# Kernel tuning notes

Hardware: AMD Instinct MI355X
Metric: run time of the kernel (lower is better)

Reference implementation:

```python
import jax, jax.numpy as jnp
import numpy as np

# Dimensions: B graphs of NPG nodes each (equal sizes -> padding == reshape, exact)
B, NPG, DIN, H, E, DOUT, K_ORDER = 8, 4096, 128, 4, 262144, 128, 4
BETA = 0.5
N = B * NPG


def setup_inputs() -> dict:
    key = jax.random.key(0)
    k = jax.random.split(key, 12)
    s = 1.0 / np.sqrt(DIN)
    so = 1.0 / np.sqrt(H * DIN)
    x = jax.random.normal(k[0], (N, DIN), jnp.float32)
    Wq_w = jax.random.normal(k[1], (H * DIN, DIN), jnp.float32) * s
    Wq_b = jax.random.normal(k[2], (H * DIN,), jnp.float32) * 0.01
    Wk_w = jax.random.normal(k[3], (H * DIN, DIN), jnp.float32) * s
    Wk_b = jax.random.normal(k[4], (H * DIN,), jnp.float32) * 0.01
    Wo_w = jax.random.normal(k[5], (DOUT, H * DIN), jnp.float32) * so
    Wo_b = jax.random.normal(k[6], (DOUT,), jnp.float32) * 0.01
    # edges constrained within graphs (faithful to per-graph data)
    g = jax.random.randint(k[7], (E,), 0, B)
    row = g * NPG + jax.random.randint(k[8], (E,), 0, NPG)
    col = g * NPG + jax.random.randint(k[9], (E,), 0, NPG)
    edge_index = jnp.stack([row, col]).astype(jnp.int32)
    n_nodes = jnp.full((B,), NPG, jnp.int32)
    return {"x": x, "Wq_w": Wq_w, "Wq_b": Wq_b, "Wk_w": Wk_w, "Wk_b": Wk_b,
            "Wo_w": Wo_w, "Wo_b": Wo_b, "edge_index": edge_index, "n_nodes": n_nodes}


def _gcn(x, row, col):
    # x: [N,H,D]; symmetric-normalized message passing via segment sums
    deg = jax.ops.segment_sum(jnp.ones(row.shape[0], x.dtype), row, num_segments=N)
    safe = jnp.where(deg > 0, deg, 1.0)
    dis = jnp.where(deg > 0, safe ** -0.5, 0.0)
    w = (dis[row] * dis[col])[:, None, None]
    return jax.ops.segment_sum(x[col] * w, row, num_segments=N)


def _attn(qs, ks, v, n_f):
    # linear attention: out_i = (q_i . sum_j k_j v_j^T + sum_j v_j) / (q_i . sum_j k_j + n)
    q4 = qs.reshape(B, NPG, H, DIN)
    k4 = ks.reshape(B, NPG, H, DIN)
    v4 = v.reshape(B, NPG, H, DIN)
    kv = jnp.einsum('bnhd,bnhe->bhde', k4, v4)          # [B,H,D,D]
    ksum = k4.sum(axis=1)                                # [B,H,D]
    vsum = v4.sum(axis=1)                                # [B,H,D]
    num = jnp.einsum('bnhd,bhde->bnhe', q4, kv) + vsum[:, None]
    den = jnp.einsum('bnhd,bhd->bnh', q4, ksum) + n_f[:, None, None]
    return (num / den[..., None]).reshape(N, H, DIN)


def reference(x, Wq_w, Wq_b, Wk_w, Wk_b, Wo_w, Wo_b, edge_index, n_nodes):
    row, col = edge_index[0], edge_index[1]
    q = (x @ Wq_w.T + Wq_b).reshape(N, H, DIN)
    k = (x @ Wk_w.T + Wk_b).reshape(N, H, DIN)
    qs = q / jnp.linalg.norm(q, axis=2, keepdims=True)
    ks = k / jnp.linalg.norm(k, axis=2, keepdims=True)
    n_f = n_nodes.astype(x.dtype)
    xh = jnp.broadcast_to(x[:, None, :], (N, H, DIN))    # repeat over heads
    acc = xh
    cur = xh
    for _ in range(K_ORDER):
        cur = BETA * _gcn(cur, row, col) + (1.0 - BETA) * _attn(qs, ks, cur, n_f)
        acc = acc + cur
    xo = acc.reshape(N, H * DIN)
    return (xo @ Wo_w.T + Wo_b) / H
```

## Files before the change

kernel.cpp:

```cpp
#include <hip/hip_runtime.h>
#include <hip/hip_bf16.h>
#include <stdint.h>

typedef __hip_bfloat16 bf16;

#define BATCH  8
#define NPG    4096
#define DIN    128
#define NH     4
#define NEDGE  262144
#define DOUTF  128
#define KORDER 4
#define NTOT   (BATCH*NPG)
#define HD     (NH*DIN)

typedef __attribute__((ext_vector_type(8))) short short8;
typedef __attribute__((ext_vector_type(4))) float f32x4;

static __device__ __forceinline__ float b2f(bf16 v) { return __bfloat162float(v); }
static __device__ __forceinline__ float u2f(unsigned short u) {
    union { float f; unsigned int i; } c; c.i = ((unsigned int)u) << 16; return c.f;
}
static __device__ __forceinline__ unsigned short f2u(float f) {
    bf16 hb = __float2bfloat16(f);
    return *(unsigned short*)&hb;
}

__global__ void zero_kernel(uint4* p, int n) {
    int i = blockIdx.x * 256 + threadIdx.x;
    if (i < n) p[i] = uint4{0u, 0u, 0u, 0u};
}

__global__ void cvtbf_kernel(const float* __restrict__ in, bf16* __restrict__ out, int n) {
    int i = (blockIdx.x * 256 + threadIdx.x) * 8;
    if (i < n) {
        float4 a = *(const float4*)(in + i);
        float4 b = *(const float4*)(in + i + 4);
        unsigned short u[8] = { f2u(a.x), f2u(a.y), f2u(a.z), f2u(a.w),
                                f2u(b.x), f2u(b.y), f2u(b.z), f2u(b.w) };
        *(uint4*)(out + i) = *(uint4*)u;
    }
}

__global__ __launch_bounds__(256) void proj_mfma_kernel(const bf16* __restrict__ xbf,
                                                        const bf16* __restrict__ Wbf,
                                                        const float* __restrict__ bias,
                                                        bf16* __restrict__ outp,
                                                        bf16* __restrict__ outT) {
    __shared__ __align__(16) short t1[32][520];
    int n0 = blockIdx.x * 32;
    int tid = threadIdx.x;
    int lane = tid & 63, wc = tid >> 6;
    int l15 = lane & 15, quad = lane >> 4;

    f32x4 acc[2][8];
    #pragma unroll
    for (int i = 0; i < 2; i++)
        #pragma unroll
        for (int j = 0; j < 8; j++) acc[i][j] = f32x4{0.f, 0.f, 0.f, 0.f};

    #pragma unroll
    for (int ks = 0; ks < 4; ks++) {
        int kk = ks * 32 + quad * 8;
        short8 af[2];
        #pragma unroll
        for (int ti = 0; ti < 2; ti++)
            af[ti] = *(const short8*)(xbf + (size_t)(n0 + ti * 16 + l15) * DIN + kk);
        #pragma unroll
        for (int tj = 0; tj < 8; tj++) {
            short8 bfr = *(const short8*)(Wbf + (size_t)(wc * 128 + tj * 16 + l15) * DIN + kk);
            acc[0][tj] = __builtin_amdgcn_mfma_f32_16x16x32_bf16(af[0], bfr, acc[0][tj], 0, 0, 0);
            acc[1][tj] = __builtin_amdgcn_mfma_f32_16x16x32_bf16(af[1], bfr, acc[1][tj], 0, 0, 0);
        }
    }

    float bias_v[8];
    #pragma unroll
    for (int tj = 0; tj < 8; tj++) bias_v[tj] = bias[wc * 128 + tj * 16 + l15];

    #pragma unroll
    for (int ti = 0; ti < 2; ti++) {
        #pragma unroll
        for (int r = 0; r < 4; r++) {
            float s = 0.f;
            #pragma unroll
            for (int tj = 0; tj < 8; tj++) {
                float v = acc[ti][tj][r] + bias_v[tj];
                acc[ti][tj][r] = v;
                s += v * v;
            }
            s += __shfl_xor(s, 1); s += __shfl_xor(s, 2);
            s += __shfl_xor(s, 4); s += __shfl_xor(s, 8);
            float rs = rsqrtf(s);
            int node = ti * 16 + quad * 4 + r;
            #pragma unroll
            for (int tj = 0; tj < 8; tj++)
                t1[node][wc * 128 + tj * 16 + l15] = (short)f2u(acc[ti][tj][r] * rs);
        }
    }
    __syncthreads();

    if (outp) {
        #pragma unroll
        for (int u = 0; u < 8; u++) {
            int unit = u * 256 + tid;
            int nl = unit >> 6, fp = (unit & 63) * 8;
            *(uint4*)(outp + (size_t)(n0 + nl) * HD + fp) = *(uint4*)&t1[nl][fp];
        }
    }
    if (outT) {
        int b = n0 >> 12, nl0 = n0 & 4095;
        #pragma unroll
        for (int u = 0; u < 8; u++) {
            int unit = u * 256 + tid;
            int f = unit >> 2, np = (unit & 3) * 8;
            unsigned short arr[8];
            #pragma unroll
            for (int j = 0; j < 8; j++) arr[j] = (unsigned short)t1[np + j][f];
            *(uint4*)(outT + ((size_t)b * HD + f) * NPG + nl0 + np) = *(uint4*)arr;
        }
    }
}

__global__ void deg_kernel(const int* __restrict__ row, int* __restrict__ deg) {
    int e = blockIdx.x * 256 + threadIdx.x;
    if (e < NEDGE) atomicAdd(&deg[row[e]], 1);
}

__global__ void dis_kernel(const int* __restrict__ deg, float* __restrict__ dis) {
    int i = blockIdx.x * 256 + threadIdx.x;
    if (i < NTOT) {
        int d = deg[i];
        dis[i] = d > 0 ? rsqrtf((float)d) : 0.f;
    }
}

__global__ __launch_bounds__(1024) void scan1_kernel(const int* __restrict__ deg,
                                                     int* __restrict__ row_ptr, int* __restrict__ bsum) {
    __shared__ int buf[1024];
    int g = blockIdx.x, t = threadIdx.x;
    int v = deg[g * 1024 + t];
    buf[t] = v;
    __syncthreads();
    for (int off = 1; off < 1024; off <<= 1) {
        int add = (t >= off) ? buf[t - off] : 0;
        __syncthreads();
        buf[t] += add;
        __syncthreads();
    }
    row_ptr[g * 1024 + t] = buf[t] - v;
    if (t == 1023) bsum[g] = buf[1023];
}

__global__ void scan2_kernel(const int* __restrict__ bsum, int* __restrict__ boff, int* __restrict__ row_ptr) {
    int run = 0;
    for (int g = 0; g < 32; g++) { boff[g] = run; run += bsum[g]; }
    row_ptr[NTOT] = run;
}

__global__ __launch_bounds__(1024) void scan3_kernel(int* __restrict__ row_ptr, const int* __restrict__ boff) {
    row_ptr[blockIdx.x * 1024 + threadIdx.x] += boff[blockIdx.x];
}

__global__ __launch_bounds__(128) void sortperm_kernel(const int* __restrict__ row_ptr,
                                                       int* __restrict__ perm) {
    __shared__ int key[128];
    __shared__ int val[128];
    int tile = blockIdx.x;
    int t = threadIdx.x;
    int n = tile * 128 + t;
    key[t] = row_ptr[n + 1] - row_ptr[n];
    val[t] = t;
    __syncthreads();
    for (int k = 2; k <= 128; k <<= 1) {
        for (int j = k >> 1; j > 0; j >>= 1) {
            int ixj = t ^ j;
            if (ixj > t) {
                int a = key[t], b = key[ixj];
                bool up = ((t & k) == 0);
                if ((a > b) == up) {
                    key[t] = b; key[ixj] = a;
                    int va = val[t]; val[t] = val[ixj]; val[ixj] = va;
                }
            }
            __syncthreads();
        }
    }
    perm[tile * 128 + t] = val[t];
}

__global__ void scatter_kernel(const int* __restrict__ row, const int* __restrict__ col,
                               const int* __restrict__ row_ptr, int* __restrict__ fill,
                               const float* __restrict__ dis,
                               uint2* __restrict__ ecw) {
    int e = blockIdx.x * 256 + threadIdx.x;
    if (e < NEDGE) {
        int r = row[e], c = col[e];
        int pos = row_ptr[r] + atomicAdd(&fill[r], 1);
        ecw[pos] = uint2{(unsigned)c, __float_as_uint(dis[c])};
    }
}

__global__ __launch_bounds__(256) void rowsum_kernel(const bf16* __restrict__ T, float* __restrict__ out) {
    int row = blockIdx.x * 4 + (threadIdx.x >> 6);
    int lane = threadIdx.x & 63;
    const ushort4* p = (const ushort4*)(T + (size_t)row * NPG);
    float s = 0.f;
    #pragma unroll
    for (int wv = 0; wv < 16; wv++) {
        ushort4 u = p[lane + wv * 64];
        s += u2f(u.x) + u2f(u.y) + u2f(u.z) + u2f(u.w);
    }
    for (int off = 32; off > 0; off >>= 1) s += __shfl_down(s, off);
    if (lane == 0) out[row] = s;
}

__global__ __launch_bounds__(256) void colsum_kernel(const bf16* __restrict__ xbf, float* __restrict__ vsum) {
    __shared__ float buf[256];
    int b = blockIdx.x >> 3, sl = blockIdx.x & 7;
    int t = threadIdx.x;
    int d = t & 127, half = t >> 7;
    const unsigned short* p = (const unsigned short*)xbf + ((size_t)b * NPG + sl * 512 + half * 256) * DIN + d;
    float s = 0.f;
    for (int r = 0; r < 256; r++) s += u2f(p[(size_t)r * DIN]);
    buf[t] = s;
    __syncthreads();
    if (half == 0) {
        float tot = buf[d] + buf[d + 128];
        #pragma unroll
        for (int h = 0; h < NH; h++) atomicAdd(&vsum[b * HD + h * DIN + d], tot);
    }
}

__global__ __launch_bounds__(256) void den_kernel(const bf16* __restrict__ qs, const float* __restrict__ ksum,
                                                  const int* __restrict__ n_nodes, float* __restrict__ rden) {
    int n = blockIdx.x;
    int b = n >> 12;
    int w = threadIdx.x >> 6, lane = threadIdx.x & 63;
    int base = w * DIN;
    float p = b2f(qs[(size_t)n * HD + base + lane])      * ksum[b * HD + base + lane]
            + b2f(qs[(size_t)n * HD + base + 64 + lane]) * ksum[b * HD + base + 64 + lane];
    for (int off = 32; off > 0; off >>= 1) p += __shfl_down(p, off);
    if (lane == 0) rden[n * NH + w] = 1.0f / (p + (float)n_nodes[b]);
}

#define KVSPLIT 16
__global__ __launch_bounds__(512, 4) void kv_mfma_kernel(const bf16* __restrict__ ksT,
                                                         const bf16* __restrict__ vsrc,
                                                         int vld, int vhm,
                                                         float* __restrict__ partial) {
    __shared__ __align__(16) short kshT[128][72];
    __shared__ __align__(16) short vshT[128][72];
    int id = blockIdx.x;
    int b = id & 7;
    int u = id >> 3;
    int h = u >> 4;
    int s = u & 15;
    int bh = b * 4 + h;
    int blk = bh * KVSPLIT + s;
    int tid = threadIdx.x;
    int lane = tid & 63;
    int w = tid >> 6;
    int wr = w >> 1, wc = w & 1;
    int d0w = wr * 32, e0w = wc * 64;
    int l15 = lane & 15, quad = lane >> 4;

    f32x4 acc[2][4];
    #pragma unroll
    for (int i = 0; i < 2; i++)
        #pragma unroll
        for (int j = 0; j < 4; j++) acc[i][j] = f32x4{0.f, 0.f, 0.f, 0.f};

    const uint4* kg = (const uint4*)(ksT + ((size_t)bh * 128) * NPG);
    const bf16* vg = vsrc + (size_t)h * vhm;
    int n0 = s * (NPG / KVSPLIT);

    for (int c = 0; c < NPG / KVSPLIT / 64; c++) {
        int nb = n0 + c * 64;
        #pragma unroll
        for (int uu = 0; uu < 2; uu++) {
            int unit = uu * 512 + tid;
            int row = unit >> 3;
            int part = unit & 7;
            uint4 kd = kg[row * (NPG / 8) + (nb >> 3) + part];
            *(uint4*)&kshT[row][part * 8] = kd;
            int nl = unit >> 4;
            int fg = unit & 15;
            uint4 vd = *(const uint4*)(vg + (size_t)(b * NPG + nb + nl) * vld + fg * 8);
            unsigned short* sv = (unsigned short*)&vd;
            int ncol = nl ^ ((fg & 7) << 3);
            #pragma unroll
            for (int j = 0; j < 8; j++) vshT[fg * 8 + j][ncol] = (short)sv[j];
        }
        __syncthreads();
        #pragma unroll
        for (int kkstep = 0; kkstep < 2; kkstep++) {
            int kk = kkstep * 32 + quad * 8;
            short8 af[2], bfr[4];
            #pragma unroll
            for (int ti = 0; ti < 2; ti++)
                af[ti] = *(const short8*)&kshT[d0w + ti * 16 + l15][kk];
            #pragma unroll
            for (int tj = 0; tj < 4; tj++) {
                int e = e0w + tj * 16 + l15;
                bfr[tj] = *(const short8*)&vshT[e][kk ^ (((e >> 3) & 7) << 3)];
            }
            #pragma unroll
            for (int ti = 0; ti < 2; ti++)
                #pragma unroll
                for (int tj = 0; tj < 4; tj++)
                    acc[ti][tj] = __builtin_amdgcn_mfma_f32_16x16x32_bf16(af[ti], bfr[tj], acc[ti][tj], 0, 0, 0);
        }
        __syncthreads();
    }
    float* p = partial + (size_t)blk * (128 * 128);
    #pragma unroll
    for (int ti = 0; ti < 2; ti++)
        #pragma unroll
        for (int tj = 0; tj < 4; tj++)
            #pragma unroll
            for (int r = 0; r < 4; r++) {
                int row = d0w + ti * 16 + quad * 4 + r;
                int col = e0w + tj * 16 + l15;
                p[row * 128 + col] = acc[ti][tj][r];
            }
}

__global__ __launch_bounds__(256) void kvredB_kernel(const float* __restrict__ partial, bf16* __restrict__ kvB) {
    __shared__ __align__(16) short t[16][136];
    int blk = blockIdx.x;
    int bh = blk >> 3;
    int e0 = (blk & 7) * 16;
    int tid = threadIdx.x;
    int el = tid & 15;
    int dc = tid >> 4;
    const float* p = partial + (size_t)bh * (KVSPLIT * 16384);
    #pragma unroll
    for (int j = 0; j < 8; j++) {
        int d = dc * 8 + j;
        int idx = d * 128 + e0 + el;
        float s = 0.f;
        #pragma unroll
        for (int sl = 0; sl < KVSPLIT; sl++) s += p[sl * 16384 + idx];
        t[el][d] = (short)f2u(s);
    }
    __syncthreads();
    int e = tid >> 4, dp = (tid & 15) * 8;
    *(uint4*)((unsigned short*)kvB + (size_t)bh * 16384 + (e0 + e) * 128 + dp) = *(uint4*)&t[e][dp];
}

static __device__ __forceinline__ void acc8(float* g, uint4 v, float w) {
    unsigned short* sv = (unsigned short*)&v;
    #pragma unroll
    for (int k = 0; k < 8; k++) g[k] += w * u2f(sv[k]);
}

#define EMAX 1536
__global__ __launch_bounds__(512, 2) void gcn_attn_kernel(const bf16* __restrict__ qs,
                                                          const bf16* __restrict__ kvB,
                                                          const bf16* __restrict__ gsrc,
                                                          int gld, int ghm,
                                                          const int* __restrict__ row_ptr,
                                                          const int* __restrict__ perm,
                                                          const uint2* __restrict__ ecw,
                                                          const float* __restrict__ dis,
                                                          const float* __restrict__ vsum,
                                                          const float* __restrict__ rden,
                                                          bf16* __restrict__ curN,
                                                          float* __restrict__ vsumN) {
    __shared__ __align__(16) short t1[128][136];
    __shared__ __align__(8) uint2 est[EMAX];
    int id = blockIdx.x;
    int b = id & 7;
    int u = id >> 3;
    int h = u >> 5;
    int m = u & 31;
    int bh = b * 4 + h;
    int n0 = b * NPG + m * 128;
    int tid = threadIdx.x;
    int lane = tid & 63, w = tid >> 6;
    int wr = w >> 1, wc = w & 1;
    int e0w = wc * 64;
    int l15 = lane & 15, quad = lane >> 4;

    int ebase = row_ptr[n0];
    int ecnt = row_ptr[n0 + 128] - ebase;
    int scnt = ecnt < EMAX ? ecnt : EMAX;
    for (int i = tid; i < scnt; i += 512) est[i] = ecw[ebase + i];
    __syncthreads();

    {
        int nl = perm[n0 + (tid >> 2)];
        int sub = tid & 3;
        int n = n0 + nl;
        int start = row_ptr[n] - ebase;
        int end   = row_ptr[n + 1] - ebase;
        int lend  = end < scnt ? end : scnt;
        float g[32];
        #pragma unroll
        for (int i = 0; i < 32; i++) g[i] = 0.f;
        const bf16* gbase = gsrc + (size_t)h * ghm + sub * 32;

        int cA = 0, cB = 0; float wA = 0.f, wB = 0.f;
        if (start < lend)     { uint2 p = est[start];     cA = (int)p.x; wA = __uint_as_float(p.y); }
        if (start + 1 < lend) { uint2 p = est[start + 1]; cB = (int)p.x; wB = __uint_as_float(p.y); }
        uint4 vA0, vA1, vA2, vA3, vB0, vB1, vB2, vB3;
        {
            const uint4* p = (const uint4*)(gbase + (size_t)cA * gld);
            vA0 = p[0]; vA1 = p[1]; vA2 = p[2]; vA3 = p[3];
        }
        {
            const uint4* p = (const uint4*)(gbase + (size_t)cB * gld);
            vB0 = p[0]; vB1 = p[1]; vB2 = p[2]; vB3 = p[3];
        }
        for (int j = start; j < lend; j += 2) {
            int cC = 0, cD = 0; float wC = 0.f, wD = 0.f;
            if (j + 2 < lend) { uint2 p = est[j + 2]; cC = (int)p.x; wC = __uint_as_float(p.y); }
            if (j + 3 < lend) { uint2 p = est[j + 3]; cD = (int)p.x; wD = __uint_as_float(p.y); }
            acc8(g +  0, vA0, wA); acc8(g +  8, vA1, wA);
            acc8(g + 16, vA2, wA); acc8(g + 24, vA3, wA);
            {
                const uint4* p = (const uint4*)(gbase + (size_t)cC * gld);
                vA0 = p[0]; vA1 = p[1]; vA2 = p[2]; vA3 = p[3];
            }
            acc8(g +  0, vB0, wB); acc8(g +  8, vB1, wB);
            acc8(g + 16, vB2, wB); acc8(g + 24, vB3, wB);
            {
                const uint4* p = (const uint4*)(gbase + (size_t)cD * gld);
                vB0 = p[0]; vB1 = p[1]; vB2 = p[2]; vB3 = p[3];
            }
            wA = wC; wB = wD;
        }
        int fstart = start > lend ? start : lend;
        for (int j = fstart; j < end; j++) {
            uint2 pe = ecw[ebase + j];
            int c = (int)pe.x; float ww = __uint_as_float(pe.y);
            const uint4* p = (const uint4*)(gbase + (size_t)c * gld);
            acc8(g +  0, p[0], ww); acc8(g +  8, p[1], ww);
            acc8(g + 16, p[2], ww); acc8(g + 24, p[3], ww);
        }

        float dn = dis[n];
        int sw = (nl >> 3) & 7;
        #pragma unroll
        for (int q = 0; q < 4; q++) {
            unsigned short arr[8];
            #pragma unroll
            for (int k = 0; k < 8; k++) arr[k] = f2u(g[q * 8 + k] * dn);
            int fb = (sub * 4 + q) ^ sw;
            *(uint4*)&t1[nl][fb * 8] = *(uint4*)arr;
        }
    }

    f32x4 acc[2][4];
    #pragma unroll
    for (int i = 0; i < 2; i++)
        #pragma unroll
        for (int j = 0; j < 4; j++) acc[i][j] = f32x4{0.f, 0.f, 0.f, 0.f};

    const bf16* Aq = qs + (size_t)n0 * HD + h * DIN;
    const unsigned short* Bk = (const unsigned short*)kvB + (size_t)bh * 16384;
    #pragma unroll
    for (int ks = 0; ks < 4; ks++) {
        int kk = ks * 32 + quad * 8;
        short8 af[2], bfr[4];
        #pragma unroll
        for (int ti = 0; ti < 2; ti++)
            af[ti] = *(const short8*)(Aq + (size_t)(wr * 32 + ti * 16 + l15) * HD + kk);
        #pragma unroll
        for (int tj = 0; tj < 4; tj++)
            bfr[tj] = *(const short8*)(Bk + (e0w + tj * 16 + l15) * 128 + kk);
        #pragma unroll
        for (int ti = 0; ti < 2; ti++)
            #pragma unroll
            for (int tj = 0; tj < 4; tj++)
                acc[ti][tj] = __builtin_amdgcn_mfma_f32_16x16x32_bf16(af[ti], bfr[tj], acc[ti][tj], 0, 0, 0);
    }
    __syncthreads();

    #pragma unroll
    for (int tj = 0; tj < 4; tj++) {
        int el = e0w + tj * 16 + l15;
        float vs = vsum[b * HD + h * DIN + el];
        float cs = 0.f;
        #pragma unroll
        for (int ti = 0; ti < 2; ti++) {
            int nlb = wr * 32 + ti * 16 + quad * 4;
            #pragma unroll
            for (int r = 0; r < 4; r++) {
                int nl = nlb + r;
                int sw = (nl >> 3) & 7;
                int pc = (((el >> 3) ^ sw) * 8) | (el & 7);
                float attnv = (acc[ti][tj][r] + vs) * rden[(size_t)(n0 + nl) * NH + h];
                float g = u2f((unsigned short)t1[nl][pc]);
                float val = 0.5f * g + 0.5f * attnv;
                t1[nl][pc] = (short)f2u(val);
                cs += val;
            }
        }
        cs += __shfl_xor(cs, 16);
        cs += __shfl_xor(cs, 32);
        if (quad == 0) atomicAdd(&vsumN[b * HD + h * DIN + el], cs);
    }
    __syncthreads();

    {
        bf16* dstn = curN + (size_t)n0 * HD + h * DIN;
        #pragma unroll
        for (int uu = 0; uu < 4; uu++) {
            int unit = uu * 512 + tid;
            int nl = unit >> 4, fb = unit & 15;
            int sw = (nl >> 3) & 7;
            uint4 v = *(uint4*)&t1[nl][(fb ^ sw) * 8];
            *(uint4*)(dstn + (size_t)nl * HD + fb * 8) = v;
        }
    }
}

__global__ __launch_bounds__(256, 4) void out_mfma_kernel(const bf16* __restrict__ xbf,
                                                          const bf16* __restrict__ c1,
                                                          const bf16* __restrict__ c2,
                                                          const bf16* __restrict__ c3,
                                                          const bf16* __restrict__ c4,
                                                          const bf16* __restrict__ Wobf,
                                                          const float* __restrict__ Wo_b,
                                                          float* __restrict__ out) {
    __shared__ __align__(16) short ash[32][520];
    int n0 = blockIdx.x * 32;
    int tid = threadIdx.x;
    int lane = tid & 63, w = tid >> 6;
    int l15 = lane & 15, quad = lane >> 4;

    #pragma unroll 4
    for (int uu = 0; uu < 8; uu++) {
        int unit = uu * 256 + tid;
        int row = unit >> 6, cg = unit & 63;
        int col = cg * 8;
        size_t rbase = (size_t)(n0 + row);
        uint4 vx = *(const uint4*)(xbf + rbase * DIN + (col & 127));
        uint4 v1 = *(const uint4*)(c1 + rbase * HD + col);
        uint4 v2 = *(const uint4*)(c2 + rbase * HD + col);
        uint4 v3 = *(const uint4*)(c3 + rbase * HD + col);
        uint4 v4 = *(const uint4*)(c4 + rbase * HD + col);
        unsigned short* px = (unsigned short*)&vx;
        unsigned short* p1 = (unsigned short*)&v1;
        unsigned short* p2 = (unsigned short*)&v2;
        unsigned short* p3 = (unsigned short*)&v3;
        unsigned short* p4 = (unsigned short*)&v4;
        unsigned short o[8];
        #pragma unroll
        for (int j = 0; j < 8; j++)
            o[j] = f2u(u2f(px[j]) + u2f(p1[j]) + u2f(p2[j]) + u2f(p3[j]) + u2f(p4[j]));
        *(uint4*)&ash[row][col] = *(uint4*)o;
    }
    __syncthreads();

    f32x4 acc[2][2];
    #pragma unroll
    for (int i = 0; i < 2; i++)
        #pragma unroll
        for (int j = 0; j < 2; j++) acc[i][j] = f32x4{0.f, 0.f, 0.f, 0.f};

    #pragma unroll
    for (int ks = 0; ks < 16; ks++) {
        int kk = ks * 32 + quad * 8;
        short8 af[2], bfr[2];
        #pragma unroll
        for (int ti = 0; ti < 2; ti++)
            af[ti] = *(const short8*)&ash[ti * 16 + l15][kk];
        #pragma unroll
        for (int tj = 0; tj < 2; tj++)
            bfr[tj] = *(const short8*)(Wobf + (size_t)(w * 32 + tj * 16 + l15) * HD + kk);
        #pragma unroll
        for (int ti = 0; ti < 2; ti++)
            #pragma unroll
            for (int tj = 0; tj < 2; tj++)
                acc[ti][tj] = __builtin_amdgcn_mfma_f32_16x16x32_bf16(af[ti], bfr[tj], acc[ti][tj], 0, 0, 0);
    }

    #pragma unroll
    for (int tj = 0; tj < 2; tj++) {
        int col = w * 32 + tj * 16 + l15;
        float bv = Wo_b[col];
        #pragma unroll
        for (int ti = 0; ti < 2; ti++) {
            int rowb = ti * 16 + quad * 4;
            #pragma unroll
            for (int r = 0; r < 4; r++)
                out[(size_t)(n0 + rowb + r) * DOUTF + col] = (acc[ti][tj][r] + bv) * 0.25f;
        }
    }
}

extern "C" void kernel_launch(void* const* d_in, const int* in_sizes, int n_in,
                              void* d_out, int out_size, void* d_ws, size_t ws_size,
                              hipStream_t stream) {
    const float* x     = (const float*)d_in[0];
    const float* Wq_w  = (const float*)d_in[1];
    const float* Wq_b  = (const float*)d_in[2];
    const float* Wk_w  = (const float*)d_in[3];
    const float* Wk_b  = (const float*)d_in[4];
    const float* Wo_w  = (const float*)d_in[5];
    const float* Wo_b  = (const float*)d_in[6];
    const int*   edge  = (const int*)d_in[7];
    const int*   n_nod = (const int*)d_in[8];
    float* out = (float*)d_out;
    const int* erow = edge;
    const int* ecol = edge + NEDGE;

    char* w = (char*)d_ws;
    auto alloc = [&](size_t bytes) -> char* {
        char* p = w;
        w += (bytes + 255) & ~(size_t)255;
        return p;
    };
    bf16*  qs      = (bf16*) alloc((size_t)NTOT * HD * 2);
    bf16*  ksT     = (bf16*) alloc((size_t)NTOT * HD * 2);
    bf16*  cur1    = (bf16*) alloc((size_t)NTOT * HD * 2);
    bf16*  cur2    = (bf16*) alloc((size_t)NTOT * HD * 2);
    bf16*  cur3    = (bf16*) alloc((size_t)NTOT * HD * 2);
    bf16*  cur4    = (bf16*) alloc((size_t)NTOT * HD * 2);
    bf16*  xbf     = (bf16*) alloc((size_t)NTOT * DIN * 2);
    float* partial = (float*)alloc((size_t)32 * KVSPLIT * 16384 * 4);
    bf16*  kvB     = (bf16*) alloc((size_t)32 * 16384 * 2);
    bf16*  Wobf    = (bf16*) alloc(DOUTF * HD * 2);
    int*   degfill = (int*)  alloc(2 * NTOT * 4);
    float* dis     = (float*)alloc(NTOT * 4);
    int*   row_ptr = (int*)  alloc((NTOT + 1) * 4);
    int*   perm    = (int*)  alloc(NTOT * 4);
    uint2* ecw     = (uint2*)alloc((size_t)NEDGE * 8);
    float* ksum    = (float*)alloc(BATCH * HD * 4);
    float* vsumA   = (float*)alloc(BATCH * HD * 4);
    float* vsumB   = (float*)alloc(BATCH * HD * 4);
    float* rden    = (float*)alloc((size_t)NTOT * NH * 4);
    int*   bsum    = (int*)  alloc(32 * 4);
    int*   boff    = (int*)  alloc(32 * 4);
    int* deg  = degfill;
    int* fill = degfill + NTOT;
    bf16* Wqbf = (bf16*)partial;
    bf16* Wkbf = Wqbf + (size_t)HD * DIN;

    zero_kernel<<<64, 256, 0, stream>>>((uint4*)degfill, 2 * NTOT / 4);

    cvtbf_kernel<<<NTOT * DIN / 8 / 256, 256, 0, stream>>>(x, xbf, NTOT * DIN);
    cvtbf_kernel<<<HD * DIN / 8 / 256, 256, 0, stream>>>(Wq_w, Wqbf, HD * DIN);
    cvtbf_kernel<<<HD * DIN / 8 / 256, 256, 0, stream>>>(Wk_w, Wkbf, HD * DIN);
    cvtbf_kernel<<<DOUTF * HD / 8 / 256, 256, 0, stream>>>(Wo_w, Wobf, DOUTF * HD);

    proj_mfma_kernel<<<NTOT / 32, 256, 0, stream>>>(xbf, Wqbf, Wq_b, qs, (bf16*)nullptr);
    proj_mfma_kernel<<<NTOT / 32, 256, 0, stream>>>(xbf, Wkbf, Wk_b, (bf16*)nullptr, ksT);

    deg_kernel<<<NEDGE / 256, 256, 0, stream>>>(erow, deg);
    dis_kernel<<<NTOT / 256, 256, 0, stream>>>(deg, dis);
    scan1_kernel<<<32, 1024, 0, stream>>>(deg, row_ptr, bsum);
    scan2_kernel<<<1, 1, 0, stream>>>(bsum, boff, row_ptr);
    scan3_kernel<<<32, 1024, 0, stream>>>(row_ptr, boff);
    sortperm_kernel<<<NTOT / 128, 128, 0, stream>>>(row_ptr, perm);
    scatter_kernel<<<NEDGE / 256, 256, 0, stream>>>(erow, ecol, row_ptr, fill, dis, ecw);

    rowsum_kernel<<<BATCH * HD / 4, 256, 0, stream>>>(ksT, ksum);
    den_kernel<<<NTOT, 256, 0, stream>>>(qs, ksum, n_nod, rden);

    zero_kernel<<<4, 256, 0, stream>>>((uint4*)vsumA, BATCH * HD / 4);
    colsum_kernel<<<64, 256, 0, stream>>>(xbf, vsumA);

    bf16* curs[4] = { cur1, cur2, cur3, cur4 };
    float* vs = vsumA;
    float* vsN = vsumB;
    for (int it = 0; it < KORDER; it++) {
        const bf16* src = (it == 0) ? xbf : curs[it - 1];
        int ld = (it == 0) ? DIN : HD;
        int hm = (it == 0) ? 0 : DIN;
        kv_mfma_kernel<<<32 * KVSPLIT, 512, 0, stream>>>(ksT, src, ld, hm, partial);
        kvredB_kernel<<<256, 256, 0, stream>>>(partial, kvB);
        zero_kernel<<<4, 256, 0, stream>>>((uint4*)vsN, BATCH * HD / 4);
        gcn_attn_kernel<<<32 * 32, 512, 0, stream>>>(qs, kvB, src, ld, hm, row_ptr, perm, ecw, dis,
                                                     vs, rden, curs[it], vsN);
        float* tf = vs; vs = vsN; vsN = tf;
    }

    out_mfma_kernel<<<NTOT / 32, 256, 0, stream>>>(xbf, cur1, cur2, cur3, cur4, Wobf, Wo_b, out);

    (void)in_sizes; (void)n_in; (void)out_size; (void)ws_size;
}
```

Baseline: 565.0 us.

## Halve gcn_attn node tile to 64 rows and fold vsum zeroing into kvred

Reworks the fused GCN+attention kernel to process 64 nodes per block instead of 128. The grid doubles to 2048 blocks, with 8 threads per node each gathering 16 features and one MFMA row-tile per wave. Sortperm and the shared edge-stage buffer shrink to match. The separate zero_kernel launch for the next vsum buffer is folded into an extra block of kvredB. The aim is more parallelism and less per-thread register pressure in the gather, plus one fewer launch per iteration, at the cost of more per-block overhead, more vsum atomics and kvB reloads.

Result: slower. 632.7 us (+12.0%).

```diff
diff --git a/kernel.cpp b/kernel.cpp
--- a/kernel.cpp
+++ b/kernel.cpp
@@ -162,17 +162,17 @@
     row_ptr[blockIdx.x * 1024 + threadIdx.x] += boff[blockIdx.x];
 }
 
-__global__ __launch_bounds__(128) void sortperm_kernel(const int* __restrict__ row_ptr,
-                                                       int* __restrict__ perm) {
-    __shared__ int key[128];
-    __shared__ int val[128];
+__global__ __launch_bounds__(64) void sortperm_kernel(const int* __restrict__ row_ptr,
+                                                      int* __restrict__ perm) {
+    __shared__ int key[64];
+    __shared__ int val[64];
     int tile = blockIdx.x;
     int t = threadIdx.x;
-    int n = tile * 128 + t;
+    int n = tile * 64 + t;
     key[t] = row_ptr[n + 1] - row_ptr[n];
     val[t] = t;
     __syncthreads();
-    for (int k = 2; k <= 128; k <<= 1) {
+    for (int k = 2; k <= 64; k <<= 1) {
         for (int j = k >> 1; j > 0; j >>= 1) {
             int ixj = t ^ j;
             if (ixj > t) {
@@ -186,7 +186,7 @@
             __syncthreads();
         }
     }
-    perm[tile * 128 + t] = val[t];
+    perm[tile * 64 + t] = val[t];
 }
 
 __global__ void scatter_kernel(const int* __restrict__ row, const int* __restrict__ col,
@@ -326,7 +326,15 @@
             }
 }
 
-__global__ __launch_bounds__(256) void kvredB_kernel(const float* __restrict__ partial, bf16* __restrict__ kvB) {
+__global__ __launch_bounds__(256) void kvredB_kernel(const float* __restrict__ partial, bf16* __restrict__ kvB,
+                                                     float* __restrict__ vsumN) {
+    if (blockIdx.x == 256) {
+        ((uint4*)vsumN)[threadIdx.x] = uint4{0u, 0u, 0u, 0u};
+        ((uint4*)vsumN)[256 + threadIdx.x] = uint4{0u, 0u, 0u, 0u};
+        ((uint4*)vsumN)[512 + threadIdx.x] = uint4{0u, 0u, 0u, 0u};
+        ((uint4*)vsumN)[768 + threadIdx.x] = uint4{0u, 0u, 0u, 0u};
+        return;
+    }
     __shared__ __align__(16) short t[16][136];
     int blk = blockIdx.x;
     int bh = blk >> 3;
@@ -355,7 +363,7 @@
     for (int k = 0; k < 8; k++) g[k] += w * u2f(sv[k]);
 }
 
-#define EMAX 1536
+#define EMAX 1024
 __global__ __launch_bounds__(512, 2) void gcn_attn_kernel(const bf16* __restrict__ qs,
                                                           const bf16* __restrict__ kvB,
                                                           const bf16* __restrict__ gsrc,
@@ -368,15 +376,15 @@
                                                           const float* __restrict__ rden,
                                                           bf16* __restrict__ curN,
                                                           float* __restrict__ vsumN) {
-    __shared__ __align__(16) short t1[128][136];
+    __shared__ __align__(16) short t1[64][136];
     __shared__ __align__(8) uint2 est[EMAX];
     int id = blockIdx.x;
     int b = id & 7;
     int u = id >> 3;
-    int h = u >> 5;
-    int m = u & 31;
+    int h = u >> 6;
+    int m = u & 63;
     int bh = b * 4 + h;
-    int n0 = b * NPG + m * 128;
+    int n0 = b * NPG + m * 64;
     int tid = threadIdx.x;
     int lane = tid & 63, w = tid >> 6;
     int wr = w >> 1, wc = w & 1;
@@ -384,50 +392,48 @@
     int l15 = lane & 15, quad = lane >> 4;
 
     int ebase = row_ptr[n0];
-    int ecnt = row_ptr[n0 + 128] - ebase;
+    int ecnt = row_ptr[n0 + 64] - ebase;
     int scnt = ecnt < EMAX ? ecnt : EMAX;
     for (int i = tid; i < scnt; i += 512) est[i] = ecw[ebase + i];
     __syncthreads();
 
     {
-        int nl = perm[n0 + (tid >> 2)];
-        int sub = tid & 3;
+        int nl = perm[n0 + (tid >> 3)];
+        int sub = tid & 7;
         int n = n0 + nl;
         int start = row_ptr[n] - ebase;
         int end   = row_ptr[n + 1] - ebase;
         int lend  = end < scnt ? end : scnt;
-        float g[32];
-        #pragma unroll
-        for (int i = 0; i < 32; i++) g[i] = 0.f;
-        const bf16* gbase = gsrc + (size_t)h * ghm + sub * 32;
+        float g[16];
+        #pragma unroll
+        for (int i = 0; i < 16; i++) g[i] = 0.f;
+        const bf16* gbase = gsrc + (size_t)h * ghm + sub * 16;
 
         int cA = 0, cB = 0; float wA = 0.f, wB = 0.f;
         if (start < lend)     { uint2 p = est[start];     cA = (int)p.x; wA = __uint_as_float(p.y); }
         if (start + 1 < lend) { uint2 p = est[start + 1]; cB = (int)p.x; wB = __uint_as_float(p.y); }
-        uint4 vA0, vA1, vA2, vA3, vB0, vB1, vB2, vB3;
+        uint4 vA0, vA1, vB0, vB1;
         {
             const uint4* p = (const uint4*)(gbase + (size_t)cA * gld);
-            vA0 = p[0]; vA1 = p[1]; vA2 = p[2]; vA3 = p[3];
+            vA0 = p[0]; vA1 = p[1];
         }
         {
             const uint4* p = (const uint4*)(gbase + (size_t)cB * gld);
-            vB0 = p[0]; vB1 = p[1]; vB2 = p[2]; vB3 = p[3];
+            vB0 = p[0]; vB1 = p[1];
         }
         for (int j = start; j < lend; j += 2) {
             int cC = 0, cD = 0; float wC = 0.f, wD = 0.f;
             if (j + 2 < lend) { uint2 p = est[j + 2]; cC = (int)p.x; wC = __uint_as_float(p.y); }
             if (j + 3 < lend) { uint2 p = est[j + 3]; cD = (int)p.x; wD = __uint_as_float(p.y); }
-            acc8(g +  0, vA0, wA); acc8(g +  8, vA1, wA);
-            acc8(g + 16, vA2, wA); acc8(g + 24, vA3, wA);
+            acc8(g + 0, vA0, wA); acc8(g + 8, vA1, wA);
             {
                 const uint4* p = (const uint4*)(gbase + (size_t)cC * gld);
-                vA0 = p[0]; vA1 = p[1]; vA2 = p[2]; vA3 = p[3];
+                vA0 = p[0]; vA1 = p[1];
             }
-            acc8(g +  0, vB0, wB); acc8(g +  8, vB1, wB);
-            acc8(g + 16, vB2, wB); acc8(g + 24, vB3, wB);
+            acc8(g + 0, vB0, wB); acc8(g + 8, vB1, wB);
             {
                 const uint4* p = (const uint4*)(gbase + (size_t)cD * gld);
-                vB0 = p[0]; vB1 = p[1]; vB2 = p[2]; vB3 = p[3];
+                vB0 = p[0]; vB1 = p[1];
             }
             wA = wC; wB = wD;
         }
@@ -436,45 +442,38 @@
             uint2 pe = ecw[ebase + j];
             int c = (int)pe.x; float ww = __uint_as_float(pe.y);
             const uint4* p = (const uint4*)(gbase + (size_t)c * gld);
-            acc8(g +  0, p[0], ww); acc8(g +  8, p[1], ww);
-            acc8(g + 16, p[2], ww); acc8(g + 24, p[3], ww);
+            acc8(g + 0, p[0], ww); acc8(g + 8, p[1], ww);
         }
 
         float dn = dis[n];
         int sw = (nl >> 3) & 7;
         #pragma unroll
-        for (int q = 0; q < 4; q++) {
+        for (int q = 0; q < 2; q++) {
             unsigned short arr[8];
             #pragma unroll
             for (int k = 0; k < 8; k++) arr[k] = f2u(g[q * 8 + k] * dn);
-            int fb = (sub * 4 + q) ^ sw;
+            int fb = (sub * 2 + q) ^ sw;
             *(uint4*)&t1[nl][fb * 8] = *(uint4*)arr;
         }
     }
 
-    f32x4 acc[2][4];
-    #pragma unroll
-    for (int i = 0; i < 2; i++)
-        #pragma unroll
-        for (int j = 0; j < 4; j++) acc[i][j] = f32x4{0.f, 0.f, 0.f, 0.f};
+    f32x4 acc[4];
+    #pragma unroll
+    for (int j = 0; j < 4; j++) acc[j] = f32x4{0.f, 0.f, 0.f, 0.f};
 
     const bf16* Aq = qs + (size_t)n0 * HD + h * DIN;
     const unsigned short* Bk = (const unsigned short*)kvB + (size_t)bh * 16384;
     #pragma unroll
     for (int ks = 0; ks < 4; ks++) {
         int kk = ks * 32 + quad * 8;
-        short8 af[2], bfr[4];
-        #pragma unroll
-        for (int ti = 0; ti < 2; ti++)
-            af[ti] = *(const short8*)(Aq + (size_t)(wr * 32 + ti * 16 + l15) * HD + kk);
+        short8 af = *(const short8*)(Aq + (size_t)(wr * 16 + l15) * HD + kk);
+        short8 bfr[4];
         #pragma unroll
         for (int tj = 0; tj < 4; tj++)
             bfr[tj] = *(const short8*)(Bk + (e0w + tj * 16 + l15) * 128 + kk);
         #pragma unroll
-        for (int ti = 0; ti < 2; ti++)
-            #pragma unroll
-            for (int tj = 0; tj < 4; tj++)
-                acc[ti][tj] = __builtin_amdgcn_mfma_f32_16x16x32_bf16(af[ti], bfr[tj], acc[ti][tj], 0, 0, 0);
+        for (int tj = 0; tj < 4; tj++)
+            acc[tj] = __builtin_amdgcn_mfma_f32_16x16x32_bf16(af, bfr[tj], acc[tj], 0, 0, 0);
     }
     __syncthreads();
 
@@ -483,20 +482,17 @@
         int el = e0w + tj * 16 + l15;
         float vs = vsum[b * HD + h * DIN + el];
         float cs = 0.f;
-        #pragma unroll
-        for (int ti = 0; ti < 2; ti++) {
-            int nlb = wr * 32 + ti * 16 + quad * 4;
-            #pragma unroll
-            for (int r = 0; r < 4; r++) {
-                int nl = nlb + r;
-                int sw = (nl >> 3) & 7;
-                int pc = (((el >> 3) ^ sw) * 8) | (el & 7);
-                float attnv = (acc[ti][tj][r] + vs) * rden[(size_t)(n0 + nl) * NH + h];
-                float g = u2f((unsigned short)t1[nl][pc]);
-                float val = 0.5f * g + 0.5f * attnv;
-                t1[nl][pc] = (short)f2u(val);
-                cs += val;
-            }
+        int nlb = wr * 16 + quad * 4;
+        #pragma unroll
+        for (int r = 0; r < 4; r++) {
+            int nl = nlb + r;
+            int sw = (nl >> 3) & 7;
+            int pc = (((el >> 3) ^ sw) * 8) | (el & 7);
+            float attnv = (acc[tj][r] + vs) * rden[(size_t)(n0 + nl) * NH + h];
+            float g = u2f((unsigned short)t1[nl][pc]);
+            float val = 0.5f * g + 0.5f * attnv;
+            t1[nl][pc] = (short)f2u(val);
+            cs += val;
         }
         cs += __shfl_xor(cs, 16);
         cs += __shfl_xor(cs, 32);
@@ -507,7 +503,7 @@
     {
         bf16* dstn = curN + (size_t)n0 * HD + h * DIN;
         #pragma unroll
-        for (int uu = 0; uu < 4; uu++) {
+        for (int uu = 0; uu < 2; uu++) {
             int unit = uu * 512 + tid;
             int nl = unit >> 4, fb = unit & 15;
             int sw = (nl >> 3) & 7;
@@ -655,7 +651,7 @@
     scan1_kernel<<<32, 1024, 0, stream>>>(deg, row_ptr, bsum);
     scan2_kernel<<<1, 1, 0, stream>>>(bsum, boff, row_ptr);
     scan3_kernel<<<32, 1024, 0, stream>>>(row_ptr, boff);
-    sortperm_kernel<<<NTOT / 128, 128, 0, stream>>>(row_ptr, perm);
+    sortperm_kernel<<<NTOT / 64, 64, 0, stream>>>(row_ptr, perm);
     scatter_kernel<<<NEDGE / 256, 256, 0, stream>>>(erow, ecol, row_ptr, fill, dis, ecw);
 
     rowsum_kernel<<<BATCH * HD / 4, 256, 0, stream>>>(ksT, ksum);
@@ -672,10 +668,9 @@
         int ld = (it == 0) ? DIN : HD;
         int hm = (it == 0) ? 0 : DIN;
         kv_mfma_kernel<<<32 * KVSPLIT, 512, 0, stream>>>(ksT, src, ld, hm, partial);
-        kvredB_kernel<<<256, 256, 0, stream>>>(partial, kvB);
-        zero_kernel<<<4, 256, 0, stream>>>((uint4*)vsN, BATCH * HD / 4);
-        gcn_attn_kernel<<<32 * 32, 512, 0, stream>>>(qs, kvB, src, ld, hm, row_ptr, perm, ecw, dis,
-                                                     vs, rden, curs[it], vsN);
+        kvredB_kernel<<<257, 256, 0, stream>>>(partial, kvB, vsN);
+        gcn_attn_kernel<<<8 * 4 * 64, 512, 0, stream>>>(qs, kvB, src, ld, hm, row_ptr, perm, ecw, dis,
+                                                        vs, rden, curs[it], vsN);
         float* tf = vs; vs = vsN; vsN = tf;
     }
 
```

## Fuse split-K KV reduction into kv_mfma via last-block atomic counter

Applied to the files above, without the earlier changes.

Removes the separate kvredB and vsum-zero kernel launches per iteration. The kv_mfma kernel now zeroes the next vsum buffer in block 0. Each block also bumps a per-(batch,head) atomic counter, and the last-arriving block reduces the 16 partials into bf16 kvB. This saves two launches per order, but the reduction now runs serially inside 32 tail blocks, each walking 8 column chunks, instead of spreading across 256 blocks.

Result: slower. 722.4 us (+27.9%).

```diff
diff --git a/kernel.cpp b/kernel.cpp
--- a/kernel.cpp
+++ b/kernel.cpp
@@ -152,9 +152,10 @@
     if (t == 1023) bsum[g] = buf[1023];
 }
 
-__global__ void scan2_kernel(const int* __restrict__ bsum, int* __restrict__ boff, int* __restrict__ row_ptr) {
+__global__ void scan2_kernel(const int* __restrict__ bsum, int* __restrict__ boff, int* __restrict__ row_ptr,
+                             int* __restrict__ cnt) {
     int run = 0;
-    for (int g = 0; g < 32; g++) { boff[g] = run; run += bsum[g]; }
+    for (int g = 0; g < 32; g++) { boff[g] = run; run += bsum[g]; cnt[g] = 0; }
     row_ptr[NTOT] = run;
 }
 
@@ -248,9 +249,13 @@
 __global__ __launch_bounds__(512, 4) void kv_mfma_kernel(const bf16* __restrict__ ksT,
                                                          const bf16* __restrict__ vsrc,
                                                          int vld, int vhm,
-                                                         float* __restrict__ partial) {
+                                                         float* __restrict__ partial,
+                                                         bf16* __restrict__ kvB,
+                                                         int* __restrict__ cnt,
+                                                         float* __restrict__ vsumN) {
     __shared__ __align__(16) short kshT[128][72];
     __shared__ __align__(16) short vshT[128][72];
+    __shared__ int isLast;
     int id = blockIdx.x;
     int b = id & 7;
     int u = id >> 3;
@@ -265,6 +270,11 @@
     int d0w = wr * 32, e0w = wc * 64;
     int l15 = lane & 15, quad = lane >> 4;
 
+    if (id == 0) {
+        ((uint4*)vsumN)[tid] = uint4{0u, 0u, 0u, 0u};
+        ((uint4*)vsumN)[512 + tid] = uint4{0u, 0u, 0u, 0u};
+    }
+
     f32x4 acc[2][4];
     #pragma unroll
     for (int i = 0; i < 2; i++)
@@ -324,29 +334,42 @@
                 int col = e0w + tj * 16 + l15;
                 p[row * 128 + col] = acc[ti][tj][r];
             }
-}
-
-__global__ __launch_bounds__(256) void kvredB_kernel(const float* __restrict__ partial, bf16* __restrict__ kvB) {
-    __shared__ __align__(16) short t[16][136];
-    int blk = blockIdx.x;
-    int bh = blk >> 3;
-    int e0 = (blk & 7) * 16;
-    int tid = threadIdx.x;
-    int el = tid & 15;
-    int dc = tid >> 4;
-    const float* p = partial + (size_t)bh * (KVSPLIT * 16384);
-    #pragma unroll
-    for (int j = 0; j < 8; j++) {
-        int d = dc * 8 + j;
-        int idx = d * 128 + e0 + el;
-        float s = 0.f;
-        #pragma unroll
-        for (int sl = 0; sl < KVSPLIT; sl++) s += p[sl * 16384 + idx];
-        t[el][d] = (short)f2u(s);
-    }
-    __syncthreads();
-    int e = tid >> 4, dp = (tid & 15) * 8;
-    *(uint4*)((unsigned short*)kvB + (size_t)bh * 16384 + (e0 + e) * 128 + dp) = *(uint4*)&t[e][dp];
+
+    __syncthreads();
+    if (tid == 0) {
+        __threadfence();
+        int old = atomicAdd(&cnt[bh], 1);
+        isLast = (old == KVSPLIT - 1);
+    }
+    __syncthreads();
+    if (!isLast) return;
+    if (tid == 0) __threadfence();
+    __syncthreads();
+
+    short (*tt)[136] = (short(*)[136])kshT;
+    const float* pp = partial + (size_t)bh * (KVSPLIT * 16384);
+    for (int e0c = 0; e0c < 8; e0c++) {
+        if (tid < 256) {
+            int el = tid & 15;
+            int dc = tid >> 4;
+            #pragma unroll
+            for (int j = 0; j < 8; j++) {
+                int d = dc * 8 + j;
+                int idx = d * 128 + e0c * 16 + el;
+                float sum = 0.f;
+                #pragma unroll
+                for (int sl = 0; sl < KVSPLIT; sl++) sum += pp[sl * 16384 + idx];
+                tt[el][d] = (short)f2u(sum);
+            }
+        }
+        __syncthreads();
+        if (tid < 256) {
+            int e = tid >> 4, dp = (tid & 15) * 8;
+            *(uint4*)((unsigned short*)kvB + (size_t)bh * 16384 + (e0c * 16 + e) * 128 + dp) = *(uint4*)&tt[e][dp];
+        }
+        __syncthreads();
+    }
+    if (tid == 0) cnt[bh] = 0;
 }
 
 static __device__ __forceinline__ void acc8(float* g, uint4 v, float w) {
@@ -635,6 +658,7 @@
     float* rden    = (float*)alloc((size_t)NTOT * NH * 4);
     int*   bsum    = (int*)  alloc(32 * 4);
     int*   boff    = (int*)  alloc(32 * 4);
+    int*   cnt     = (int*)  alloc(32 * 4);
     int* deg  = degfill;
     int* fill = degfill + NTOT;
     bf16* Wqbf = (bf16*)partial;
@@ -653,7 +677,7 @@
     deg_kernel<<<NEDGE / 256, 256, 0, stream>>>(erow, deg);
     dis_kernel<<<NTOT / 256, 256, 0, stream>>>(deg, dis);
     scan1_kernel<<<32, 1024, 0, stream>>>(deg, row_ptr, bsum);
-    scan2_kernel<<<1, 1, 0, stream>>>(bsum, boff, row_ptr);
+    scan2_kernel<<<1, 1, 0, stream>>>(bsum, boff, row_ptr, cnt);
     scan3_kernel<<<32, 1024, 0, stream>>>(row_ptr, boff);
     sortperm_kernel<<<NTOT / 128, 128, 0, stream>>>(row_ptr, perm);
     scatter_kernel<<<NEDGE / 256, 256, 0, stream>>>(erow, ecol, row_ptr, fill, dis, ecw);
@@ -671,9 +695,7 @@
         const bf16* src = (it == 0) ? xbf : curs[it - 1];
         int ld = (it == 0) ? DIN : HD;
         int hm = (it == 0) ? 0 : DIN;
-        kv_mfma_kernel<<<32 * KVSPLIT, 512, 0, stream>>>(ksT, src, ld, hm, partial);
-        kvredB_kernel<<<256, 256, 0, stream>>>(partial, kvB);
-        zero_kernel<<<4, 256, 0, stream>>>((uint4*)vsN, BATCH * HD / 4);
+        kv_mfma_kernel<<<32 * KVSPLIT, 512, 0, stream>>>(ksT, src, ld, hm, partial, kvB, cnt, vsN);
         gcn_attn_kernel<<<32 * 32, 512, 0, stream>>>(qs, kvB, src, ld, hm, row_ptr, perm, ecw, dis,
                                                      vs, rden, curs[it], vsN);
         float* tf = vs; vs = vsN; vsN = tf;
```
